# Kernel tuning notes

Hardware: AMD Instinct MI355X
Metric: run time of the kernel (lower is better)

The kernel has to match this reference:

```python
import jax, jax.numpy as jnp
import numpy as np

B, N, H = 2, 8192, 128
EPS = 1e-06


def setup_inputs() -> dict:
    key = jax.random.key(0)
    k1, k2, k3, k4 = jax.random.split(key, 4)
    x = jax.random.normal(k1, (B, N, H), dtype=jnp.float32)
    # adjacency is sparse in the original (tf.sparse); represented dense here
    # for the reference math (same result as sparse_dense_matmul).
    adj = jax.random.normal(k2, (B, N, N), dtype=jnp.float32)
    W = jax.random.normal(k3, (H, H), dtype=jnp.float32)
    b = jax.random.normal(k4, (H,), dtype=jnp.float32)
    return {"x": x, "adj": adj, "W": W, "b": b}


def reference(x, adj, W, b):
    # in-degree over |adj|, per batch, per node: [B, N]
    in_degrees = jnp.sum(jnp.abs(adj), axis=-1)
    # symmetric-ish degree normalization: [B, N, 1]
    norm = jnp.power(in_degrees + EPS, -0.5)[..., None]
    # dense projection: [B, N, H]
    support = jnp.matmul(x, W)
    # batched SpMM (dense equivalent) with pre/post degree norm
    out = jnp.einsum("bmn,bnh->bmh", adj, support * norm) * norm
    return jax.nn.elu(out + b)
```

## Files before the change

### kernel.cpp

```cpp
#include <hip/hip_runtime.h>
#include <hip/hip_bf16.h>
#include <math.h>

#define NN 8192
#define HD 128
#define NB 2
#define EPSF 1e-6f
#define BM 64
#define BK 128
#define NSTEP (NN / BK)

typedef __attribute__((ext_vector_type(8))) __bf16 bf16x8;
typedef __attribute__((ext_vector_type(4))) float f32x4;

__global__ __launch_bounds__(256) void k_degree(const float* __restrict__ adj,
                                                float* __restrict__ norm) {
    const int row  = blockIdx.x * 4 + (threadIdx.x >> 6);
    const int lane = threadIdx.x & 63;
    const float4* p = (const float4*)(adj + (size_t)row * NN);
    float s = 0.f;
#pragma unroll
    for (int i = 0; i < 32; ++i) {
        float4 v = p[(size_t)i * 64 + lane];
        s += fabsf(v.x) + fabsf(v.y) + fabsf(v.z) + fabsf(v.w);
    }
#pragma unroll
    for (int off = 32; off > 0; off >>= 1) s += __shfl_down(s, off);
    if (lane == 0) norm[row] = rsqrtf(s + EPSF);
}

__global__ __launch_bounds__(256) void k_support(const float* __restrict__ x,
                                                 const float* __restrict__ W,
                                                 const float* __restrict__ norm,
                                                 __hip_bfloat16* __restrict__ snT2) {
    const int b  = blockIdx.x >> 9;
    const int n0 = (blockIdx.x & 511) * 16;
    __shared__ float xs[16][132];
    const int t = threadIdx.x;
    {
        const int r = t >> 4, c0 = (t & 15) * 8;
        const float* src = x + ((size_t)(b * NN + n0 + r)) * HD + c0;
        *(float4*)&xs[r][c0]     = *(const float4*)src;
        *(float4*)&xs[r][c0 + 4] = *(const float4*)(src + 4);
    }
    __syncthreads();
    const int nl = t & 15;
    const int h0 = (t >> 4) * 8;
    float s[8] = {0.f,0.f,0.f,0.f,0.f,0.f,0.f,0.f};
#pragma unroll 4
    for (int k = 0; k < HD; ++k) {
        const float xv = xs[nl][k];
        const float* wr = W + k * HD + h0;
        float4 wa = *(const float4*)wr;
        float4 wb = *(const float4*)(wr + 4);
        s[0] += xv * wa.x; s[1] += xv * wa.y; s[2] += xv * wa.z; s[3] += xv * wa.w;
        s[4] += xv * wb.x; s[5] += xv * wb.y; s[6] += xv * wb.z; s[7] += xv * wb.w;
    }
    const int n  = n0 + nl;
    const float nv = norm[b * NN + n];
    __hip_bfloat16* dst = snT2 + (size_t)b * NN * HD
                        + (size_t)(n >> 5) * (HD * 32) + (n & 31);
#pragma unroll
    for (int hb = 0; hb < 8; ++hb)
        dst[(h0 + hb) * 32] = __float2bfloat16(s[hb] * nv);
}

__device__ __forceinline__ bf16x8 cvt8(float4 a, float4 b) {
    bf16x8 r;
    r[0] = (__bf16)a.x; r[1] = (__bf16)a.y; r[2] = (__bf16)a.z; r[3] = (__bf16)a.w;
    r[4] = (__bf16)b.x; r[5] = (__bf16)b.y; r[6] = (__bf16)b.z; r[7] = (__bf16)b.w;
    return r;
}

__device__ __forceinline__ void gload_lds16(const float* g, void* l) {
    __builtin_amdgcn_global_load_lds(
        (const __attribute__((address_space(1))) void*)g,
        (__attribute__((address_space(3))) void*)l, 16, 0, 0);
}

__global__ __launch_bounds__(512, 2) void k_gemm17(const float* __restrict__ adj,
                                                   const __hip_bfloat16* __restrict__ snT2,
                                                   const float* __restrict__ norm,
                                                   const float* __restrict__ bias,
                                                   float* __restrict__ out) {
    const int b    = blockIdx.y;
    const int swz  = (blockIdx.x & 7) * 16 + (blockIdx.x >> 3);
    const int m0   = swz * BM;
    const int w    = threadIdx.x >> 6;
    const int mh   = w & 1;
    const int hs   = w >> 1;
    const int lane = threadIdx.x & 63;
    const int fr   = lane & 15;
    const int g    = lane >> 4;
    const int xr   = fr & 7;

    const float* adjB = adj + (size_t)b * NN * NN;
    const __hip_bfloat16* snB = snT2 + (size_t)b * NN * HD;

    __shared__ __align__(16) char Abuf[4][BM * BK * 4];

    const float* sptr[4];
#pragma unroll
    for (int c = 0; c < 4; ++c) {
        const int fg   = c * 512 + w * 64 + lane;
        const int row  = fg >> 5;
        const int gsrc = (fg & 31) ^ (row & 7);
        sptr[c] = adjB + (size_t)(m0 + row) * NN + gsrc * 4;
    }

    const __hip_bfloat16* bp0 = snB + (size_t)(hs * 32 + fr) * 32 + g * 8;
    const __hip_bfloat16* bp1 = bp0 + 16 * 32;

    f32x4 acc[2][2] = {};
    bf16x8 BfA[2][4], BfB[2][4];

#define STAGE(idx) do {                                                       \
        char* nb_ = Abuf[(idx) & 3];                                          \
        _Pragma("unroll")                                                     \
        for (int c = 0; c < 4; ++c)                                           \
            gload_lds16(sptr[c] + (idx) * BK, &nb_[c * 8192 + w * 1024]);     \
    } while (0)
#define LOADB(BX, idx) do {                                                   \
        _Pragma("unroll")                                                     \
        for (int ks = 0; ks < 4; ++ks) {                                      \
            const size_t kp_ = (size_t)((idx) * 4 + ks) * (HD * 32);          \
            BX[0][ks] = *(const bf16x8*)(bp0 + kp_);                          \
            BX[1][ks] = *(const bf16x8*)(bp1 + kp_);                          \
        }                                                                     \
    } while (0)
#define WAITN(n) asm volatile("s_waitcnt vmcnt(" #n ")" ::: "memory")
#define BAR() do { __builtin_amdgcn_s_barrier();                              \
                   __builtin_amdgcn_sched_barrier(0); } while (0)
#define COMPUTE(kidx, BX) do {                                                \
        const char* lb_ = Abuf[(kidx) & 3];                                   \
        _Pragma("unroll")                                                     \
        for (int mt = 0; mt < 2; ++mt) {                                      \
            const char* rbase_ = lb_ + (mh * 32 + mt * 16 + fr) * 512;        \
            _Pragma("unroll")                                                 \
            for (int ks = 0; ks < 4; ++ks) {                                  \
                float4 fa_ = *(const float4*)(rbase_ + ((ks * 8 + ((g * 2 + 0) ^ xr)) << 4)); \
                float4 fb_ = *(const float4*)(rbase_ + ((ks * 8 + ((g * 2 + 1) ^ xr)) << 4)); \
                bf16x8 af_ = cvt8(fa_, fb_);                                  \
                acc[mt][0] = __builtin_amdgcn_mfma_f32_16x16x32_bf16(af_, BX[0][ks], acc[mt][0], 0, 0, 0); \
                acc[mt][1] = __builtin_amdgcn_mfma_f32_16x16x32_bf16(af_, BX[1][ks], acc[mt][1], 0, 0, 0); \
            }                                                                 \
        }                                                                     \
    } while (0)

    STAGE(0);
    STAGE(1);
    LOADB(BfA, 0);

#pragma unroll 1
    for (int k = 0; k < NSTEP - 3; k += 2) {
        LOADB(BfB, k + 1);
        STAGE(k + 2);
        WAITN(16); BAR();
        COMPUTE(k, BfA);

        LOADB(BfA, k + 2);
        STAGE(k + 3);
        WAITN(16); BAR();
        COMPUTE(k + 1, BfB);
    }

    LOADB(BfB, NSTEP - 1);
    WAITN(0); BAR();
    COMPUTE(NSTEP - 2, BfA);

    WAITN(0); BAR();
    COMPUTE(NSTEP - 1, BfB);

#undef STAGE
#undef LOADB
#undef WAITN
#undef BAR
#undef COMPUTE

    const float* normB = norm + b * NN + m0;
    float* outB = out + ((size_t)b * NN + m0) * HD;
#pragma unroll
    for (int mt = 0; mt < 2; ++mt)
#pragma unroll
        for (int ht = 0; ht < 2; ++ht) {
            const int h  = hs * 32 + ht * 16 + fr;
            const float bv = bias[h];
#pragma unroll
            for (int j = 0; j < 4; ++j) {
                const int r = mh * 32 + mt * 16 + g * 4 + j;
                float v = acc[mt][ht][j] * normB[r] + bv;
                v = v > 0.f ? v : expm1f(v);
                outB[(size_t)r * HD + h] = v;
            }
        }
}

extern "C" void kernel_launch(void* const* d_in, const int* in_sizes, int n_in,
                              void* d_out, int out_size, void* d_ws, size_t ws_size,
                              hipStream_t stream) {
    (void)in_sizes; (void)n_in; (void)out_size; (void)ws_size;
    const float* x    = (const float*)d_in[0];
    const float* adj  = (const float*)d_in[1];
    const float* W    = (const float*)d_in[2];
    const float* bias = (const float*)d_in[3];
    float* out = (float*)d_out;

    float* norm = (float*)d_ws;
    __hip_bfloat16* snT2 = (__hip_bfloat16*)((char*)d_ws + 65536);

    k_degree <<<dim3(NB * NN / 4),  dim3(256), 0, stream>>>(adj, norm);
    k_support<<<dim3(NB * NN / 16), dim3(256), 0, stream>>>(x, W, norm, snT2);
    k_gemm17 <<<dim3(NN / BM, NB),  dim3(512), 0, stream>>>(adj, snT2, norm, bias, out);
}
```

Measured before the change: 236.2 us.

## Cast adjacency to bf16 in the degree pass and stream bf16 into the GEMM

The degree kernel now also writes a bf16 copy of the adjacency into workspace. The GEMM stages that bf16 copy through LDS with a doubled K tile (256) instead of staging fp32 and converting in registers. This is meant to halve the bytes the GEMM reads and to drop the per-fragment fp32-to-bf16 conversion. In exchange it adds a 256 MB write in the first pass, so total DRAM traffic stays about the same. It also drops the occupancy hint from 2 to 1 and needs a large workspace.

```diff
diff --git a/kernel.cpp b/kernel.cpp
--- a/kernel.cpp
+++ b/kernel.cpp
@@ -7,22 +7,32 @@
 #define NB 2
 #define EPSF 1e-6f
 #define BM 64
-#define BK 128
-#define NSTEP (NN / BK)
+#define BKE 256
+#define NSTEP (NN / BKE)
 
 typedef __attribute__((ext_vector_type(8))) __bf16 bf16x8;
+typedef __attribute__((ext_vector_type(4))) __bf16 bf16x4;
 typedef __attribute__((ext_vector_type(4))) float f32x4;
 
-__global__ __launch_bounds__(256) void k_degree(const float* __restrict__ adj,
-                                                float* __restrict__ norm) {
+__global__ __launch_bounds__(256) void k_degcast(const float* __restrict__ adj,
+                                                 float* __restrict__ norm,
+                                                 __hip_bfloat16* __restrict__ adjh) {
     const int row  = blockIdx.x * 4 + (threadIdx.x >> 6);
     const int lane = threadIdx.x & 63;
     const float4* p = (const float4*)(adj + (size_t)row * NN);
+    bf16x4* q = (bf16x4*)(adjh + (size_t)row * NN);
     float s = 0.f;
 #pragma unroll
-    for (int i = 0; i < 32; ++i) {
-        float4 v = p[(size_t)i * 64 + lane];
-        s += fabsf(v.x) + fabsf(v.y) + fabsf(v.z) + fabsf(v.w);
+    for (int i = 0; i < 16; ++i) {
+        float4 a = p[i * 128 + lane];
+        float4 b = p[i * 128 + 64 + lane];
+        s += fabsf(a.x) + fabsf(a.y) + fabsf(a.z) + fabsf(a.w)
+           + fabsf(b.x) + fabsf(b.y) + fabsf(b.z) + fabsf(b.w);
+        bf16x4 ha, hb;
+        ha[0] = (__bf16)a.x; ha[1] = (__bf16)a.y; ha[2] = (__bf16)a.z; ha[3] = (__bf16)a.w;
+        hb[0] = (__bf16)b.x; hb[1] = (__bf16)b.y; hb[2] = (__bf16)b.z; hb[3] = (__bf16)b.w;
+        q[i * 128 + lane]      = ha;
+        q[i * 128 + 64 + lane] = hb;
     }
 #pragma unroll
     for (int off = 32; off > 0; off >>= 1) s += __shfl_down(s, off);
@@ -65,20 +75,13 @@
         dst[(h0 + hb) * 32] = __float2bfloat16(s[hb] * nv);
 }
 
-__device__ __forceinline__ bf16x8 cvt8(float4 a, float4 b) {
-    bf16x8 r;
-    r[0] = (__bf16)a.x; r[1] = (__bf16)a.y; r[2] = (__bf16)a.z; r[3] = (__bf16)a.w;
-    r[4] = (__bf16)b.x; r[5] = (__bf16)b.y; r[6] = (__bf16)b.z; r[7] = (__bf16)b.w;
-    return r;
-}
-
-__device__ __forceinline__ void gload_lds16(const float* g, void* l) {
+__device__ __forceinline__ void gload_lds16(const void* g, void* l) {
     __builtin_amdgcn_global_load_lds(
         (const __attribute__((address_space(1))) void*)g,
         (__attribute__((address_space(3))) void*)l, 16, 0, 0);
 }
 
-__global__ __launch_bounds__(512, 2) void k_gemm17(const float* __restrict__ adj,
+__global__ __launch_bounds__(512, 1) void k_gemm18(const __hip_bfloat16* __restrict__ adjh,
                                                    const __hip_bfloat16* __restrict__ snT2,
                                                    const float* __restrict__ norm,
                                                    const float* __restrict__ bias,
@@ -94,36 +97,36 @@
     const int g    = lane >> 4;
     const int xr   = fr & 7;
 
-    const float* adjB = adj + (size_t)b * NN * NN;
-    const __hip_bfloat16* snB = snT2 + (size_t)b * NN * HD;
-
-    __shared__ __align__(16) char Abuf[4][BM * BK * 4];
-
-    const float* sptr[4];
+    const __hip_bfloat16* adjB = adjh + (size_t)b * NN * NN;
+    const __hip_bfloat16* snB  = snT2 + (size_t)b * NN * HD;
+
+    __shared__ __align__(16) char Abuf[4][BM * BKE * 2];
+
+    const __hip_bfloat16* sptr[4];
 #pragma unroll
     for (int c = 0; c < 4; ++c) {
         const int fg   = c * 512 + w * 64 + lane;
         const int row  = fg >> 5;
-        const int gsrc = (fg & 31) ^ (row & 7);
-        sptr[c] = adjB + (size_t)(m0 + row) * NN + gsrc * 4;
+        const int slot = (fg & 31) ^ (row & 7);
+        sptr[c] = adjB + (size_t)(m0 + row) * NN + slot * 8;
     }
 
     const __hip_bfloat16* bp0 = snB + (size_t)(hs * 32 + fr) * 32 + g * 8;
     const __hip_bfloat16* bp1 = bp0 + 16 * 32;
 
     f32x4 acc[2][2] = {};
-    bf16x8 BfA[2][4], BfB[2][4];
+    bf16x8 BfA[2][8], BfB[2][8];
 
 #define STAGE(idx) do {                                                       \
         char* nb_ = Abuf[(idx) & 3];                                          \
         _Pragma("unroll")                                                     \
         for (int c = 0; c < 4; ++c)                                           \
-            gload_lds16(sptr[c] + (idx) * BK, &nb_[c * 8192 + w * 1024]);     \
+            gload_lds16(sptr[c] + (size_t)(idx) * BKE, &nb_[c * 8192 + w * 1024]); \
     } while (0)
 #define LOADB(BX, idx) do {                                                   \
         _Pragma("unroll")                                                     \
-        for (int ks = 0; ks < 4; ++ks) {                                      \
-            const size_t kp_ = (size_t)((idx) * 4 + ks) * (HD * 32);          \
+        for (int ks = 0; ks < 8; ++ks) {                                      \
+            const size_t kp_ = (size_t)((idx) * 8 + ks) * (HD * 32);          \
             BX[0][ks] = *(const bf16x8*)(bp0 + kp_);                          \
             BX[1][ks] = *(const bf16x8*)(bp1 + kp_);                          \
         }                                                                     \
@@ -137,10 +140,8 @@
         for (int mt = 0; mt < 2; ++mt) {                                      \
             const char* rbase_ = lb_ + (mh * 32 + mt * 16 + fr) * 512;        \
             _Pragma("unroll")                                                 \
-            for (int ks = 0; ks < 4; ++ks) {                                  \
-                float4 fa_ = *(const float4*)(rbase_ + ((ks * 8 + ((g * 2 + 0) ^ xr)) << 4)); \
-                float4 fb_ = *(const float4*)(rbase_ + ((ks * 8 + ((g * 2 + 1) ^ xr)) << 4)); \
-                bf16x8 af_ = cvt8(fa_, fb_);                                  \
+            for (int ks = 0; ks < 8; ++ks) {                                  \
+                bf16x8 af_ = *(const bf16x8*)(rbase_ + (((ks * 4 + g) ^ xr) << 4)); \
                 acc[mt][0] = __builtin_amdgcn_mfma_f32_16x16x32_bf16(af_, BX[0][ks], acc[mt][0], 0, 0, 0); \
                 acc[mt][1] = __builtin_amdgcn_mfma_f32_16x16x32_bf16(af_, BX[1][ks], acc[mt][1], 0, 0, 0); \
             }                                                                 \
@@ -155,12 +156,12 @@
     for (int k = 0; k < NSTEP - 3; k += 2) {
         LOADB(BfB, k + 1);
         STAGE(k + 2);
-        WAITN(16); BAR();
+        WAITN(24); BAR();
         COMPUTE(k, BfA);
 
         LOADB(BfA, k + 2);
         STAGE(k + 3);
-        WAITN(16); BAR();
+        WAITN(24); BAR();
         COMPUTE(k + 1, BfB);
     }
 
@@ -207,8 +208,9 @@
 
     float* norm = (float*)d_ws;
     __hip_bfloat16* snT2 = (__hip_bfloat16*)((char*)d_ws + 65536);
-
-    k_degree <<<dim3(NB * NN / 4),  dim3(256), 0, stream>>>(adj, norm);
+    __hip_bfloat16* adjh = (__hip_bfloat16*)((char*)d_ws + 65536 + (4 << 20));
+
+    k_degcast<<<dim3(NB * NN / 4),  dim3(256), 0, stream>>>(adj, norm, adjh);
     k_support<<<dim3(NB * NN / 16), dim3(256), 0, stream>>>(x, W, norm, snT2);
-    k_gemm17 <<<dim3(NN / BM, NB),  dim3(512), 0, stream>>>(adj, snT2, norm, bias, out);
-}
+    k_gemm18 <<<dim3(NN / BM, NB),  dim3(512), 0, stream>>>(adjh, snT2, norm, bias, out);
+}
```

Result: slower. 266.3 us (+12.7%).

## Split GEMM K dimension in two with separate finalize kernel for epilogue

Applied to the files above, without the earlier changes.

The adjacency GEMM is split along K into two halves, doubling the block count from 256 to 512, halving BK to 64 and raising the occupancy hint to 4 blocks per CU. Each block writes raw partial accumulators to workspace, and a new elementwise kernel sums the two partials and applies norm, bias and ELU. The aim is better CU utilisation and latency hiding on a memory-bound GEMM. The cost is an extra kernel launch and an 8 MB partials round trip.

```diff
diff --git a/kernel.cpp b/kernel.cpp
--- a/kernel.cpp
+++ b/kernel.cpp
@@ -7,8 +7,10 @@
 #define NB 2
 #define EPSF 1e-6f
 #define BM 64
-#define BK 128
-#define NSTEP (NN / BK)
+#define BK 64
+#define KSPL 2
+#define KCH (NN / KSPL)
+#define NSTEP (KCH / BK)
 
 typedef __attribute__((ext_vector_type(8))) __bf16 bf16x8;
 typedef __attribute__((ext_vector_type(4))) float f32x4;
@@ -78,14 +80,15 @@
         (__attribute__((address_space(3))) void*)l, 16, 0, 0);
 }
 
-__global__ __launch_bounds__(512, 2) void k_gemm17(const float* __restrict__ adj,
+__global__ __launch_bounds__(512, 4) void k_gemm19(const float* __restrict__ adj,
                                                    const __hip_bfloat16* __restrict__ snT2,
-                                                   const float* __restrict__ norm,
-                                                   const float* __restrict__ bias,
-                                                   float* __restrict__ out) {
+                                                   float* __restrict__ partials) {
     const int b    = blockIdx.y;
-    const int swz  = (blockIdx.x & 7) * 16 + (blockIdx.x >> 3);
-    const int m0   = swz * BM;
+    const int swz  = (blockIdx.x & 7) * 32 + (blockIdx.x >> 3);
+    const int mb   = swz >> 1;
+    const int ksp  = swz & 1;
+    const int m0   = mb * BM;
+    const int kb   = ksp * KCH;
     const int w    = threadIdx.x >> 6;
     const int mh   = w & 1;
     const int hs   = w >> 1;
@@ -99,31 +102,32 @@
 
     __shared__ __align__(16) char Abuf[4][BM * BK * 4];
 
-    const float* sptr[4];
-#pragma unroll
-    for (int c = 0; c < 4; ++c) {
+    const float* sptr[2];
+#pragma unroll
+    for (int c = 0; c < 2; ++c) {
         const int fg   = c * 512 + w * 64 + lane;
-        const int row  = fg >> 5;
-        const int gsrc = (fg & 31) ^ (row & 7);
-        sptr[c] = adjB + (size_t)(m0 + row) * NN + gsrc * 4;
-    }
-
-    const __hip_bfloat16* bp0 = snB + (size_t)(hs * 32 + fr) * 32 + g * 8;
+        const int row  = fg >> 4;
+        const int slot = (fg & 15) ^ (row & 7);
+        sptr[c] = adjB + (size_t)(m0 + row) * NN + kb + slot * 4;
+    }
+
+    const __hip_bfloat16* bp0 = snB + (size_t)ksp * 128 * (HD * 32)
+                              + (size_t)(hs * 32 + fr) * 32 + g * 8;
     const __hip_bfloat16* bp1 = bp0 + 16 * 32;
 
     f32x4 acc[2][2] = {};
-    bf16x8 BfA[2][4], BfB[2][4];
+    bf16x8 BfA[2][2], BfB[2][2];
 
 #define STAGE(idx) do {                                                       \
         char* nb_ = Abuf[(idx) & 3];                                          \
         _Pragma("unroll")                                                     \
-        for (int c = 0; c < 4; ++c)                                           \
-            gload_lds16(sptr[c] + (idx) * BK, &nb_[c * 8192 + w * 1024]);     \
+        for (int c = 0; c < 2; ++c)                                           \
+            gload_lds16(sptr[c] + (size_t)(idx) * BK, &nb_[c * 8192 + w * 1024]); \
     } while (0)
 #define LOADB(BX, idx) do {                                                   \
         _Pragma("unroll")                                                     \
-        for (int ks = 0; ks < 4; ++ks) {                                      \
-            const size_t kp_ = (size_t)((idx) * 4 + ks) * (HD * 32);          \
+        for (int ks = 0; ks < 2; ++ks) {                                      \
+            const size_t kp_ = (size_t)((idx) * 2 + ks) * (HD * 32);          \
             BX[0][ks] = *(const bf16x8*)(bp0 + kp_);                          \
             BX[1][ks] = *(const bf16x8*)(bp1 + kp_);                          \
         }                                                                     \
@@ -135,9 +139,9 @@
         const char* lb_ = Abuf[(kidx) & 3];                                   \
         _Pragma("unroll")                                                     \
         for (int mt = 0; mt < 2; ++mt) {                                      \
-            const char* rbase_ = lb_ + (mh * 32 + mt * 16 + fr) * 512;        \
+            const char* rbase_ = lb_ + (mh * 32 + mt * 16 + fr) * 256;        \
             _Pragma("unroll")                                                 \
-            for (int ks = 0; ks < 4; ++ks) {                                  \
+            for (int ks = 0; ks < 2; ++ks) {                                  \
                 float4 fa_ = *(const float4*)(rbase_ + ((ks * 8 + ((g * 2 + 0) ^ xr)) << 4)); \
                 float4 fb_ = *(const float4*)(rbase_ + ((ks * 8 + ((g * 2 + 1) ^ xr)) << 4)); \
                 bf16x8 af_ = cvt8(fa_, fb_);                                  \
@@ -155,12 +159,12 @@
     for (int k = 0; k < NSTEP - 3; k += 2) {
         LOADB(BfB, k + 1);
         STAGE(k + 2);
-        WAITN(16); BAR();
+        WAITN(8); BAR();
         COMPUTE(k, BfA);
 
         LOADB(BfA, k + 2);
         STAGE(k + 3);
-        WAITN(16); BAR();
+        WAITN(8); BAR();
         COMPUTE(k + 1, BfB);
     }
 
@@ -177,22 +181,48 @@
 #undef BAR
 #undef COMPUTE
 
-    const float* normB = norm + b * NN + m0;
-    float* outB = out + ((size_t)b * NN + m0) * HD;
+    float* pb = partials + ((((size_t)b * 128 + mb) * 2 + ksp) << 13);
 #pragma unroll
     for (int mt = 0; mt < 2; ++mt)
 #pragma unroll
         for (int ht = 0; ht < 2; ++ht) {
-            const int h  = hs * 32 + ht * 16 + fr;
-            const float bv = bias[h];
+            const int h = hs * 32 + ht * 16 + fr;
 #pragma unroll
             for (int j = 0; j < 4; ++j) {
                 const int r = mh * 32 + mt * 16 + g * 4 + j;
-                float v = acc[mt][ht][j] * normB[r] + bv;
-                v = v > 0.f ? v : expm1f(v);
-                outB[(size_t)r * HD + h] = v;
+                pb[r * 128 + h] = acc[mt][ht][j];
             }
         }
+}
+
+__global__ __launch_bounds__(256) void k_fin(const float* __restrict__ partials,
+                                             const float* __restrict__ norm,
+                                             const float* __restrict__ bias,
+                                             float* __restrict__ out) {
+    const int f = blockIdx.x * 256 + threadIdx.x;
+    const size_t e = (size_t)f * 4;
+    const int b   = (int)(e >> 20);
+    const int rem = (int)(e & 1048575);
+    const int m   = rem >> 7;
+    const int h   = rem & 127;
+    const int mb  = m >> 6;
+    const int r   = m & 63;
+    const size_t base = (((size_t)b * 128 + mb) * 2) << 13;
+    const int off = r * 128 + h;
+    float4 p0 = *(const float4*)(partials + base + off);
+    float4 p1 = *(const float4*)(partials + base + 8192 + off);
+    const float nm = norm[b * NN + m];
+    float4 bv = *(const float4*)(bias + h);
+    float4 o;
+    o.x = (p0.x + p1.x) * nm + bv.x;
+    o.y = (p0.y + p1.y) * nm + bv.y;
+    o.z = (p0.z + p1.z) * nm + bv.z;
+    o.w = (p0.w + p1.w) * nm + bv.w;
+    o.x = o.x > 0.f ? o.x : expm1f(o.x);
+    o.y = o.y > 0.f ? o.y : expm1f(o.y);
+    o.z = o.z > 0.f ? o.z : expm1f(o.z);
+    o.w = o.w > 0.f ? o.w : expm1f(o.w);
+    *(float4*)(out + e) = o;
 }
 
 extern "C" void kernel_launch(void* const* d_in, const int* in_sizes, int n_in,
@@ -207,8 +237,10 @@
 
     float* norm = (float*)d_ws;
     __hip_bfloat16* snT2 = (__hip_bfloat16*)((char*)d_ws + 65536);
+    float* partials = (float*)((char*)d_ws + 65536 + (4 << 20));
 
     k_degree <<<dim3(NB * NN / 4),  dim3(256), 0, stream>>>(adj, norm);
     k_support<<<dim3(NB * NN / 16), dim3(256), 0, stream>>>(x, W, norm, snT2);
-    k_gemm17 <<<dim3(NN / BM, NB),  dim3(512), 0, stream>>>(adj, snT2, norm, bias, out);
-}
+    k_gemm19 <<<dim3(256, NB),      dim3(512), 0, stream>>>(adj, snT2, partials);
+    k_fin    <<<dim3(2048),         dim3(256), 0, stream>>>(partials, norm, bias, out);
+}
```

New measurement: 259.1 us. +9.7%, slower.
